# Kernel optimization log

Measured on AMD Instinct MI355X. Metric: run time of the kernel, lower is better.

Reference implementation:

```python
import jax, jax.numpy as jnp
import numpy as np

# ROIAlign config (torchvision semantics, aligned=False)
SPATIAL_SCALE = 0.25
POOLED = 7
SAMPLING_RATIO = 2
MODE = "max"  # from __init__ mode='max'


def setup_inputs() -> dict:
    key = jax.random.key(0)
    kf, kcx, kcy, kw, kh, kb = jax.random.split(key, 6)
    B, C, H, W = 2, 256, 200, 304
    N = 512
    IMG_H, IMG_W = H / SPATIAL_SCALE, W / SPATIAL_SCALE
    feature = jax.random.normal(kf, (B, C, H, W), dtype=jnp.float32)
    cx = jax.random.uniform(kcx, (N,)) * IMG_W
    cy = jax.random.uniform(kcy, (N,)) * IMG_H
    bw = jax.random.uniform(kw, (N,)) * 192.0 + 16.0
    bh = jax.random.uniform(kh, (N,)) * 192.0 + 16.0
    x1 = jnp.clip(cx - bw * 0.5, 0.0, IMG_W - 2.0)
    y1 = jnp.clip(cy - bh * 0.5, 0.0, IMG_H - 2.0)
    x2 = jnp.clip(cx + bw * 0.5, x1 + 1.0, IMG_W - 1.0)
    y2 = jnp.clip(cy + bh * 0.5, y1 + 1.0, IMG_H - 1.0)
    boxes = jnp.stack([x1, y1, x2, y2], axis=1).astype(jnp.float32)
    batch_idx = jax.random.randint(kb, (N,), 0, B, dtype=jnp.int32)
    return {"feature": feature, "boxes": boxes, "batch_idx": batch_idx}


def _sample_coords(start, size):
    # start,size: [N]; returns [N, POOLED*SAMPLING_RATIO] sample coordinates
    bin_sz = size / POOLED                         # [N]
    p = jnp.arange(POOLED, dtype=jnp.float32)      # bin index
    s = (jnp.arange(SAMPLING_RATIO, dtype=jnp.float32) + 0.5) / SAMPLING_RATIO
    # coord = start + (p + s) * bin_sz  -> [N, POOLED, RATIO]
    c = start[:, None, None] + (p[None, :, None] + s[None, None, :]) * bin_sz[:, None, None]
    return c.reshape(c.shape[0], POOLED * SAMPLING_RATIO)


def roi_align(feature, boxes, batch_idx):
    B, C, H, W = feature.shape
    roi = boxes * SPATIAL_SCALE                    # [N,4] in feature coords
    rs_x, rs_y, re_x, re_y = roi[:, 0], roi[:, 1], roi[:, 2], roi[:, 3]
    roi_w = jnp.maximum(re_x - rs_x, 1.0)
    roi_h = jnp.maximum(re_y - rs_y, 1.0)
    ys = _sample_coords(rs_y, roi_h)               # [N, Sy]
    xs = _sample_coords(rs_x, roi_w)               # [N, Sx]
    y = jnp.broadcast_to(ys[:, :, None], (ys.shape[0], ys.shape[1], xs.shape[1]))
    x = jnp.broadcast_to(xs[:, None, :], y.shape)  # [N, Sy, Sx]

    valid = (y > -1.0) & (y < H) & (x > -1.0) & (x < W)
    y = jnp.clip(y, 0.0, H - 1)
    x = jnp.clip(x, 0.0, W - 1)
    y0 = jnp.floor(y).astype(jnp.int32)
    x0 = jnp.floor(x).astype(jnp.int32)
    y1 = jnp.minimum(y0 + 1, H - 1)
    x1 = jnp.minimum(x0 + 1, W - 1)
    ly = y - y0.astype(y.dtype)
    lx = x - x0.astype(x.dtype)
    hy, hx = 1.0 - ly, 1.0 - lx
    b = batch_idx[:, None, None]
    # advanced indexing -> [N, Sy, Sx, C]
    val = (hy * hx)[..., None] * feature[b, :, y0, x0] \
        + (hy * lx)[..., None] * feature[b, :, y0, x1] \
        + (ly * hx)[..., None] * feature[b, :, y1, x0] \
        + (ly * lx)[..., None] * feature[b, :, y1, x1]
    val = jnp.where(valid[..., None], val, 0.0)
    N = boxes.shape[0]
    val = val.reshape(N, POOLED, SAMPLING_RATIO, POOLED, SAMPLING_RATIO, C)
    if MODE == "max":
        out = val.max(axis=(2, 4))                 # [N, PH, PW, C]
    else:
        out = val.mean(axis=(2, 4))
    return jnp.transpose(out, (0, 3, 1, 2))        # [N, C, PH, PW]


def reference(feature, boxes, batch_idx):
    return roi_align(feature, boxes, batch_idx)
```

## Files before the change

kernel.cpp:

```cpp
#include <hip/hip_runtime.h>


#define SPATIAL_SCALE 0.25f
#define POOLED 7
#define SR 2

constexpr int Bc = 2;
constexpr int Cc = 256;
constexpr int Hc = 200;
constexpr int Wc = 304;
constexpr int Nc = 512;

constexpr int CG      = 4;
constexpr int NSAMP   = POOLED * SR;
constexpr int NROW    = NSAMP * 2;
constexpr int XW      = 64;
constexpr int XPAD    = 68;
constexpr int CH_STR  = NROW * XPAD;
constexpr int CELLS   = POOLED * POOLED;
constexpr int OUTS    = CG * CELLS;
constexpr int PER_BOX = Cc * CELLS;
constexpr int PLANE   = Hc * Wc;

__global__ __launch_bounds__(256) void roi_align_max_kernel(
    const float* __restrict__ feature,
    const float* __restrict__ boxes,
    const int*   __restrict__ batch_idx,
    float*       __restrict__ out)
{
    __shared__ float lds[CG * CH_STR];

    int bid = blockIdx.x;
    int cg  = bid / Nc;
    int n   = bid - cg * Nc;
    int tid = threadIdx.x;

    float rsx = boxes[n * 4 + 0] * SPATIAL_SCALE;
    float rsy = boxes[n * 4 + 1] * SPATIAL_SCALE;
    float rex = boxes[n * 4 + 2] * SPATIAL_SCALE;
    float rey = boxes[n * 4 + 3] * SPATIAL_SCALE;
    float roi_w = fmaxf(rex - rsx, 1.0f);
    float roi_h = fmaxf(rey - rsy, 1.0f);
    float bin_w = roi_w / (float)POOLED;
    float bin_h = roi_h / (float)POOLED;
    int b = batch_idx[n];

    float x_first = __fadd_rn(rsx, __fmul_rn(0.25f, bin_w));
    float xc0 = fminf(fmaxf(x_first, 0.0f), (float)(Wc - 1));
    int xbase = ((int)floorf(xc0)) & ~3;

    const float* __restrict__ gbase =
        feature + ((size_t)b * Cc + (size_t)cg * CG) * (size_t)PLANE;

    int lane16 = tid & 15;
    int rbase  = tid >> 4;
    #pragma unroll
    for (int it = 0; it < 7; ++it) {
        int r       = it * 16 + rbase;
        int c_local = r / NROW;
        int slot    = r - c_local * NROW;
        int s       = slot >> 1;
        int which   = slot & 1;
        int p       = s >> 1;
        int sub     = s & 1;
        float py = (float)p + ((float)sub + 0.5f) * 0.5f;
        float fy = __fadd_rn(rsy, __fmul_rn(py, bin_h));
        float fyc = fminf(fmaxf(fy, 0.0f), (float)(Hc - 1));
        int y0 = (int)floorf(fyc);
        int row = which ? min(y0 + 1, Hc - 1) : y0;

        int col = xbase + lane16 * 4;
        col = min(col, Wc - 4);
        const float4 v = *(const float4*)(gbase + (size_t)c_local * PLANE
                                          + row * Wc + col);
        *(float4*)&lds[c_local * CH_STR + slot * XPAD + lane16 * 4] = v;
    }
    __syncthreads();

    if (tid < OUTS) {
        int c_local = tid / CELLS;
        int cell    = tid - c_local * CELLS;
        int ph      = cell / POOLED;
        int pw      = cell - ph * POOLED;
        const float* __restrict__ L = &lds[c_local * CH_STR];

        float m = -INFINITY;
        #pragma unroll
        for (int sy = 0; sy < SR; ++sy) {
            int sY = ph * SR + sy;
            float py = (float)ph + ((float)sy + 0.5f) * 0.5f;
            float fy = __fadd_rn(rsy, __fmul_rn(py, bin_h));
            bool vy = (fy > -1.0f) && (fy < (float)Hc);
            float fyc = fminf(fmaxf(fy, 0.0f), (float)(Hc - 1));
            int y0 = (int)floorf(fyc);
            float ly = fyc - (float)y0;
            float hy = 1.0f - ly;
            const float* __restrict__ r0 = L + (2 * sY) * XPAD;
            const float* __restrict__ r1 = L + (2 * sY + 1) * XPAD;

            #pragma unroll
            for (int sx = 0; sx < SR; ++sx) {
                float px = (float)pw + ((float)sx + 0.5f) * 0.5f;
                float fx = __fadd_rn(rsx, __fmul_rn(px, bin_w));
                bool vx = (fx > -1.0f) && (fx < (float)Wc);
                float fxc = fminf(fmaxf(fx, 0.0f), (float)(Wc - 1));
                int x0 = (int)floorf(fxc);
                float lx = fxc - (float)x0;
                float hx = 1.0f - lx;
                int c0 = x0 - xbase;
                int x1 = min(x0 + 1, Wc - 1);
                int c1 = x1 - xbase;

                float v00 = r0[c0], v01 = r0[c1];
                float v10 = r1[c0], v11 = r1[c1];
                float bil = hy * hx * v00 + hy * lx * v01 +
                            ly * hx * v10 + ly * lx * v11;
                float v = (vy && vx) ? bil : 0.0f;
                m = fmaxf(m, v);
            }
        }
        out[(size_t)n * PER_BOX + cg * OUTS + tid] = m;
    }
}

extern "C" void kernel_launch(void* const* d_in, const int* in_sizes, int n_in,
                              void* d_out, int out_size, void* d_ws, size_t ws_size,
                              hipStream_t stream) {
    const float* feature   = (const float*)d_in[0];
    const float* boxes     = (const float*)d_in[1];
    const int*   batch_idx = (const int*)d_in[2];
    float*       out       = (float*)d_out;

    int grid = (Cc / CG) * Nc;
    roi_align_max_kernel<<<grid, 256, 0, stream>>>(feature, boxes, batch_idx, out);
}
```

Before: 228.5 us.

## Loop channel groups per block with register-prefetched feature rows and precomputed weights

Each block now handles one box across 8 channel groups in a loop instead of one channel group, cutting the grid from one block per (box, channel group) to one per (box, chunk). The next group's feature rows are prefetched into registers while the current group is reduced from shared memory. Per-thread bilinear weights, validity masks and shared-memory addresses are computed once and reused across groups. Outputs use nontemporal stores. The gains come from amortising box setup and overlapping global loads with compute, at the cost of more registers, fewer blocks and an extra barrier per iteration.

```diff
diff --git a/kernel.cpp b/kernel.cpp
--- a/kernel.cpp
+++ b/kernel.cpp
@@ -21,6 +21,9 @@
 constexpr int OUTS    = CG * CELLS;
 constexpr int PER_BOX = Cc * CELLS;
 constexpr int PLANE   = Hc * Wc;
+constexpr int NCHUNK  = 8;
+constexpr int JITER   = (Cc / CG) / NCHUNK;
+constexpr int JSTEP_PLANES = NCHUNK * CG;
 
 __global__ __launch_bounds__(256) void roi_align_max_kernel(
     const float* __restrict__ feature,
@@ -30,96 +33,138 @@
 {
     __shared__ float lds[CG * CH_STR];
 
-    int bid = blockIdx.x;
-    int cg  = bid / Nc;
-    int n   = bid - cg * Nc;
-    int tid = threadIdx.x;
+    const int bid   = blockIdx.x;
+    const int chunk = bid & (NCHUNK - 1);
+    const int n     = bid >> 3;
+    const int tid   = threadIdx.x;
 
-    float rsx = boxes[n * 4 + 0] * SPATIAL_SCALE;
-    float rsy = boxes[n * 4 + 1] * SPATIAL_SCALE;
-    float rex = boxes[n * 4 + 2] * SPATIAL_SCALE;
-    float rey = boxes[n * 4 + 3] * SPATIAL_SCALE;
-    float roi_w = fmaxf(rex - rsx, 1.0f);
-    float roi_h = fmaxf(rey - rsy, 1.0f);
-    float bin_w = roi_w / (float)POOLED;
-    float bin_h = roi_h / (float)POOLED;
-    int b = batch_idx[n];
+    const float rsx = boxes[n * 4 + 0] * SPATIAL_SCALE;
+    const float rsy = boxes[n * 4 + 1] * SPATIAL_SCALE;
+    const float rex = boxes[n * 4 + 2] * SPATIAL_SCALE;
+    const float rey = boxes[n * 4 + 3] * SPATIAL_SCALE;
+    const float roi_w = fmaxf(rex - rsx, 1.0f);
+    const float roi_h = fmaxf(rey - rsy, 1.0f);
+    const float bin_w = roi_w / (float)POOLED;
+    const float bin_h = roi_h / (float)POOLED;
+    const int   b     = batch_idx[n];
 
-    float x_first = __fadd_rn(rsx, __fmul_rn(0.25f, bin_w));
-    float xc0 = fminf(fmaxf(x_first, 0.0f), (float)(Wc - 1));
-    int xbase = ((int)floorf(xc0)) & ~3;
+    const float x_first = __fadd_rn(rsx, __fmul_rn(0.25f, bin_w));
+    const float xc0     = fminf(fmaxf(x_first, 0.0f), (float)(Wc - 1));
+    const int   xbase   = ((int)floorf(xc0)) & ~3;
 
-    const float* __restrict__ gbase =
-        feature + ((size_t)b * Cc + (size_t)cg * CG) * (size_t)PLANE;
+    const int c_st   = tid >> 6;
+    const int lane   = tid & 63;
+    const int lane16 = lane & 15;
+    const int rquad  = lane >> 4;
 
-    int lane16 = tid & 15;
-    int rbase  = tid >> 4;
+    int g_off[7];
     #pragma unroll
     for (int it = 0; it < 7; ++it) {
-        int r       = it * 16 + rbase;
-        int c_local = r / NROW;
-        int slot    = r - c_local * NROW;
-        int s       = slot >> 1;
-        int which   = slot & 1;
-        int p       = s >> 1;
-        int sub     = s & 1;
-        float py = (float)p + ((float)sub + 0.5f) * 0.5f;
-        float fy = __fadd_rn(rsy, __fmul_rn(py, bin_h));
-        float fyc = fminf(fmaxf(fy, 0.0f), (float)(Hc - 1));
-        int y0 = (int)floorf(fyc);
-        int row = which ? min(y0 + 1, Hc - 1) : y0;
-
+        const int slot  = it * 4 + rquad;
+        const int s     = slot % NSAMP;
+        const int which = slot / NSAMP;
+        const int p     = s >> 1;
+        const int sub   = s & 1;
+        const float py  = (float)p + ((float)sub + 0.5f) * 0.5f;
+        const float fy  = __fadd_rn(rsy, __fmul_rn(py, bin_h));
+        const float fyc = fminf(fmaxf(fy, 0.0f), (float)(Hc - 1));
+        const int   y0  = (int)floorf(fyc);
+        const int   row = which ? min(y0 + 1, Hc - 1) : y0;
         int col = xbase + lane16 * 4;
         col = min(col, Wc - 4);
-        const float4 v = *(const float4*)(gbase + (size_t)c_local * PLANE
-                                          + row * Wc + col);
-        *(float4*)&lds[c_local * CH_STR + slot * XPAD + lane16 * 4] = v;
+        g_off[it] = row * Wc + col;
     }
-    __syncthreads();
+    const int lw = c_st * CH_STR + rquad * XPAD + lane16 * 4;
 
-    if (tid < OUTS) {
-        int c_local = tid / CELLS;
-        int cell    = tid - c_local * CELLS;
-        int ph      = cell / POOLED;
-        int pw      = cell - ph * POOLED;
-        const float* __restrict__ L = &lds[c_local * CH_STR];
+    const float* gp = feature
+        + ((size_t)b * Cc + (size_t)chunk * CG + c_st) * (size_t)PLANE;
 
-        float m = -INFINITY;
+    const bool has_out = (tid < OUTS);
+    float w00[2][2], w01[2][2], w10[2][2], w11[2][2];
+    int   adr[2][2][2];
+    float* outp = nullptr;
+
+    if (has_out) {
+        const int c_cl = tid / CELLS;
+        const int cell = tid - c_cl * CELLS;
+        const int ph   = cell / POOLED;
+        const int pw   = cell - ph * POOLED;
+
         #pragma unroll
         for (int sy = 0; sy < SR; ++sy) {
-            int sY = ph * SR + sy;
-            float py = (float)ph + ((float)sy + 0.5f) * 0.5f;
-            float fy = __fadd_rn(rsy, __fmul_rn(py, bin_h));
-            bool vy = (fy > -1.0f) && (fy < (float)Hc);
-            float fyc = fminf(fmaxf(fy, 0.0f), (float)(Hc - 1));
-            int y0 = (int)floorf(fyc);
-            float ly = fyc - (float)y0;
-            float hy = 1.0f - ly;
-            const float* __restrict__ r0 = L + (2 * sY) * XPAD;
-            const float* __restrict__ r1 = L + (2 * sY + 1) * XPAD;
+            const int   sY  = ph * SR + sy;
+            const float py  = (float)ph + ((float)sy + 0.5f) * 0.5f;
+            const float fy  = __fadd_rn(rsy, __fmul_rn(py, bin_h));
+            const bool  vy  = (fy > -1.0f) && (fy < (float)Hc);
+            const float fyc = fminf(fmaxf(fy, 0.0f), (float)(Hc - 1));
+            const int   y0i = (int)floorf(fyc);
+            const float ly  = fyc - (float)y0i;
+            const float hy  = 1.0f - ly;
 
             #pragma unroll
             for (int sx = 0; sx < SR; ++sx) {
-                float px = (float)pw + ((float)sx + 0.5f) * 0.5f;
-                float fx = __fadd_rn(rsx, __fmul_rn(px, bin_w));
-                bool vx = (fx > -1.0f) && (fx < (float)Wc);
-                float fxc = fminf(fmaxf(fx, 0.0f), (float)(Wc - 1));
-                int x0 = (int)floorf(fxc);
-                float lx = fxc - (float)x0;
-                float hx = 1.0f - lx;
-                int c0 = x0 - xbase;
-                int x1 = min(x0 + 1, Wc - 1);
-                int c1 = x1 - xbase;
-
-                float v00 = r0[c0], v01 = r0[c1];
-                float v10 = r1[c0], v11 = r1[c1];
-                float bil = hy * hx * v00 + hy * lx * v01 +
-                            ly * hx * v10 + ly * lx * v11;
-                float v = (vy && vx) ? bil : 0.0f;
-                m = fmaxf(m, v);
+                const float px  = (float)pw + ((float)sx + 0.5f) * 0.5f;
+                const float fx  = __fadd_rn(rsx, __fmul_rn(px, bin_w));
+                const bool  vx  = (fx > -1.0f) && (fx < (float)Wc);
+                const float fxc = fminf(fmaxf(fx, 0.0f), (float)(Wc - 1));
+                const int   x0i = (int)floorf(fxc);
+                const float lx  = fxc - (float)x0i;
+                const float hx  = 1.0f - lx;
+                const int   c0  = x0i - xbase;
+                const bool  v   = vy && vx;
+                w00[sy][sx] = v ? hy * hx : 0.0f;
+                w01[sy][sx] = v ? hy * lx : 0.0f;
+                w10[sy][sx] = v ? ly * hx : 0.0f;
+                w11[sy][sx] = v ? ly * lx : 0.0f;
+                adr[sy][0][sx] = c_cl * CH_STR + sY * XPAD + c0;
+                adr[sy][1][sx] = c_cl * CH_STR + (sY + NSAMP) * XPAD + c0;
             }
         }
-        out[(size_t)n * PER_BOX + cg * OUTS + tid] = m;
+        outp = out + (size_t)n * PER_BOX
+                   + ((size_t)chunk * CG + c_cl) * CELLS + cell;
+    }
+
+    float4 st[7];
+    #pragma unroll
+    for (int it = 0; it < 7; ++it)
+        st[it] = *(const float4*)(gp + g_off[it]);
+
+    for (int j = 0; j < JITER; ++j) {
+        #pragma unroll
+        for (int it = 0; it < 7; ++it)
+            *(float4*)&lds[lw + it * (4 * XPAD)] = st[it];
+
+        if (j + 1 < JITER) {
+            gp += (size_t)JSTEP_PLANES * PLANE;
+            #pragma unroll
+            for (int it = 0; it < 7; ++it)
+                st[it] = *(const float4*)(gp + g_off[it]);
+        }
+
+        __syncthreads();
+
+        if (has_out) {
+            float m = -INFINITY;
+            #pragma unroll
+            for (int sy = 0; sy < SR; ++sy) {
+                #pragma unroll
+                for (int sx = 0; sx < SR; ++sx) {
+                    const int a0 = adr[sy][0][sx];
+                    const int a1 = adr[sy][1][sx];
+                    const float v00 = lds[a0];
+                    const float v01 = lds[a0 + 1];
+                    const float v10 = lds[a1];
+                    const float v11 = lds[a1 + 1];
+                    const float bil = w00[sy][sx] * v00 + w01[sy][sx] * v01
+                                    + w10[sy][sx] * v10 + w11[sy][sx] * v11;
+                    m = fmaxf(m, bil);
+                }
+            }
+            __builtin_nontemporal_store(m, outp);
+            outp += NCHUNK * CG * CELLS;
+        }
+
+        __syncthreads();
     }
 }
 
@@ -131,6 +176,6 @@
     const int*   batch_idx = (const int*)d_in[2];
     float*       out       = (float*)d_out;
 
-    int grid = (Cc / CG) * Nc;
+    int grid = Nc * NCHUNK;
     roi_align_max_kernel<<<grid, 256, 0, stream>>>(feature, boxes, batch_idx, out);
 }
```

After: 513.5 us. +124.7%, slower.

## Precompute per-ROI bilinear weights and LDS offsets in a separate kernel

Applied to the files above, without the earlier changes.

Adds a small precompute kernel that writes, for each box, the bilinear weights (with the validity mask folded in), the LDS tap offsets, the row offsets and xbase into a workspace table. The main kernel reads this table instead of recomputing the coordinates in every one of the 64 channel-group blocks per box. It also restructures the staging loads so each thread issues all 7 global float4 loads before any LDS stores, and changes the LDS row layout. The cost is an extra kernel launch and table reads, and the workspace must be large enough, otherwise a fallback kernel runs.

```diff
diff --git a/kernel.cpp b/kernel.cpp
--- a/kernel.cpp
+++ b/kernel.cpp
@@ -14,7 +14,6 @@
 constexpr int CG      = 4;
 constexpr int NSAMP   = POOLED * SR;
 constexpr int NROW    = NSAMP * 2;
-constexpr int XW      = 64;
 constexpr int XPAD    = 68;
 constexpr int CH_STR  = NROW * XPAD;
 constexpr int CELLS   = POOLED * POOLED;
@@ -22,7 +21,160 @@
 constexpr int PER_BOX = Cc * CELLS;
 constexpr int PLANE   = Hc * Wc;
 
-__global__ __launch_bounds__(256) void roi_align_max_kernel(
+constexpr int TB_F  = 1216;
+constexpr int A_OFF = 784;
+constexpr int R_OFF = 1176;
+constexpr int X_OFF = 1204;
+constexpr size_t TABLE_BYTES = (size_t)Nc * TB_F * sizeof(float);
+
+__global__ __launch_bounds__(64) void roi_precompute_kernel(
+    const float* __restrict__ boxes,
+    float*       __restrict__ table)
+{
+    const int n   = blockIdx.x;
+    const int tid = threadIdx.x;
+
+    const float rsx = boxes[n * 4 + 0] * SPATIAL_SCALE;
+    const float rsy = boxes[n * 4 + 1] * SPATIAL_SCALE;
+    const float rex = boxes[n * 4 + 2] * SPATIAL_SCALE;
+    const float rey = boxes[n * 4 + 3] * SPATIAL_SCALE;
+    const float roi_w = fmaxf(rex - rsx, 1.0f);
+    const float roi_h = fmaxf(rey - rsy, 1.0f);
+    const float bin_w = roi_w / (float)POOLED;
+    const float bin_h = roi_h / (float)POOLED;
+    const float x_first = __fadd_rn(rsx, __fmul_rn(0.25f, bin_w));
+    const float xc0     = fminf(fmaxf(x_first, 0.0f), (float)(Wc - 1));
+    const int   xbase   = ((int)floorf(xc0)) & ~3;
+
+    float* tb = table + (size_t)n * TB_F;
+    int*   ti = (int*)tb;
+
+    if (tid < CELLS) {
+        const int ph = tid / POOLED;
+        const int pw = tid - ph * POOLED;
+        #pragma unroll
+        for (int sy = 0; sy < SR; ++sy) {
+            const int   sY  = ph * SR + sy;
+            const float py  = (float)ph + ((float)sy + 0.5f) * 0.5f;
+            const float fy  = __fadd_rn(rsy, __fmul_rn(py, bin_h));
+            const bool  vy  = (fy > -1.0f) && (fy < (float)Hc);
+            const float fyc = fminf(fmaxf(fy, 0.0f), (float)(Hc - 1));
+            const int   y0i = (int)floorf(fyc);
+            const float ly  = fyc - (float)y0i;
+            const float hy  = 1.0f - ly;
+            #pragma unroll
+            for (int sx = 0; sx < SR; ++sx) {
+                const float px  = (float)pw + ((float)sx + 0.5f) * 0.5f;
+                const float fx  = __fadd_rn(rsx, __fmul_rn(px, bin_w));
+                const bool  vx  = (fx > -1.0f) && (fx < (float)Wc);
+                const float fxc = fminf(fmaxf(fx, 0.0f), (float)(Wc - 1));
+                const int   x0i = (int)floorf(fxc);
+                const float lx  = fxc - (float)x0i;
+                const float hx  = 1.0f - lx;
+                const int   c0  = x0i - xbase;
+                const bool  v   = vy && vx;
+                float4 w;
+                w.x = v ? hy * hx : 0.0f;
+                w.y = v ? hy * lx : 0.0f;
+                w.z = v ? ly * hx : 0.0f;
+                w.w = v ? ly * lx : 0.0f;
+                const int tap = sy * SR + sx;
+                ((float4*)tb)[tid * 4 + tap] = w;
+                ti[A_OFF + tid * 8 + tap * 2 + 0] = sY * XPAD + c0;
+                ti[A_OFF + tid * 8 + tap * 2 + 1] = (NSAMP + sY) * XPAD + c0;
+            }
+        }
+    }
+    if (tid < NROW) {
+        const int which = tid / NSAMP;
+        const int s     = tid - which * NSAMP;
+        const int p     = s >> 1;
+        const int sub   = s & 1;
+        const float py  = (float)p + ((float)sub + 0.5f) * 0.5f;
+        const float fy  = __fadd_rn(rsy, __fmul_rn(py, bin_h));
+        const float fyc = fminf(fmaxf(fy, 0.0f), (float)(Hc - 1));
+        const int   y0  = (int)floorf(fyc);
+        const int   row = which ? min(y0 + 1, Hc - 1) : y0;
+        ti[R_OFF + tid] = row * Wc;
+    }
+    if (tid == 0) ti[X_OFF] = xbase;
+}
+
+__global__ __launch_bounds__(256) void roi_align_main_kernel(
+    const float* __restrict__ feature,
+    const int*   __restrict__ batch_idx,
+    const float* __restrict__ table,
+    float*       __restrict__ out)
+{
+    __shared__ float lds[CG * CH_STR];
+
+    const int bid = blockIdx.x;
+    const int cg  = bid / Nc;
+    const int n   = bid - cg * Nc;
+    const int tid = threadIdx.x;
+
+    const float* tb = table + (size_t)n * TB_F;
+    const int*   ti = (const int*)tb;
+
+    const int b     = batch_idx[n];
+    const int xbase = ti[X_OFF];
+
+    const int c_st   = tid >> 6;
+    const int lane16 = tid & 15;
+    const int rquad  = (tid >> 4) & 3;
+    const int col    = min(xbase + lane16 * 4, Wc - 4);
+
+    int roff[7];
+    #pragma unroll
+    for (int it = 0; it < 7; ++it)
+        roff[it] = ti[R_OFF + it * 4 + rquad];
+
+    const int cellc = min(tid, OUTS - 1);
+    const int c_cl  = cellc / CELLS;
+    const int cell  = cellc - c_cl * CELLS;
+    const float4* wp = (const float4*)tb + (size_t)cell * 4;
+    const float4 wv0 = wp[0], wv1 = wp[1], wv2 = wp[2], wv3 = wp[3];
+    const int4* ap = (const int4*)(ti + A_OFF) + (size_t)cell * 2;
+    const int4 av0 = ap[0], av1 = ap[1];
+
+    const float* __restrict__ gbase =
+        feature + ((size_t)b * Cc + (size_t)cg * CG + c_st) * (size_t)PLANE;
+    float4 st[7];
+    #pragma unroll
+    for (int it = 0; it < 7; ++it)
+        st[it] = *(const float4*)(gbase + roff[it] + col);
+
+    const int lw = c_st * CH_STR + rquad * XPAD + lane16 * 4;
+    #pragma unroll
+    for (int it = 0; it < 7; ++it)
+        *(float4*)&lds[lw + it * (4 * XPAD)] = st[it];
+
+    __syncthreads();
+
+    if (tid < OUTS) {
+        const int lbase = c_cl * CH_STR;
+        float m = -INFINITY;
+        {   const int a0 = av0.x + lbase, a1 = av0.y + lbase;
+            const float bil = wv0.x * lds[a0] + wv0.y * lds[a0 + 1]
+                            + wv0.z * lds[a1] + wv0.w * lds[a1 + 1];
+            m = fmaxf(m, bil); }
+        {   const int a0 = av0.z + lbase, a1 = av0.w + lbase;
+            const float bil = wv1.x * lds[a0] + wv1.y * lds[a0 + 1]
+                            + wv1.z * lds[a1] + wv1.w * lds[a1 + 1];
+            m = fmaxf(m, bil); }
+        {   const int a0 = av1.x + lbase, a1 = av1.y + lbase;
+            const float bil = wv2.x * lds[a0] + wv2.y * lds[a0 + 1]
+                            + wv2.z * lds[a1] + wv2.w * lds[a1 + 1];
+            m = fmaxf(m, bil); }
+        {   const int a0 = av1.z + lbase, a1 = av1.w + lbase;
+            const float bil = wv3.x * lds[a0] + wv3.y * lds[a0 + 1]
+                            + wv3.z * lds[a1] + wv3.w * lds[a1 + 1];
+            m = fmaxf(m, bil); }
+        out[(size_t)n * PER_BOX + cg * OUTS + tid] = m;
+    }
+}
+
+__global__ __launch_bounds__(256) void roi_align_max_fallback(
     const float* __restrict__ feature,
     const float* __restrict__ boxes,
     const int*   __restrict__ batch_idx,
@@ -59,8 +211,8 @@
         int r       = it * 16 + rbase;
         int c_local = r / NROW;
         int slot    = r - c_local * NROW;
-        int s       = slot >> 1;
-        int which   = slot & 1;
+        int s       = slot % NSAMP;
+        int which   = slot / NSAMP;
         int p       = s >> 1;
         int sub     = s & 1;
         float py = (float)p + ((float)sub + 0.5f) * 0.5f;
@@ -68,11 +220,9 @@
         float fyc = fminf(fmaxf(fy, 0.0f), (float)(Hc - 1));
         int y0 = (int)floorf(fyc);
         int row = which ? min(y0 + 1, Hc - 1) : y0;
-
-        int col = xbase + lane16 * 4;
-        col = min(col, Wc - 4);
+        int colf = min(xbase + lane16 * 4, Wc - 4);
         const float4 v = *(const float4*)(gbase + (size_t)c_local * PLANE
-                                          + row * Wc + col);
+                                          + row * Wc + colf);
         *(float4*)&lds[c_local * CH_STR + slot * XPAD + lane16 * 4] = v;
     }
     __syncthreads();
@@ -95,8 +245,8 @@
             int y0 = (int)floorf(fyc);
             float ly = fyc - (float)y0;
             float hy = 1.0f - ly;
-            const float* __restrict__ r0 = L + (2 * sY) * XPAD;
-            const float* __restrict__ r1 = L + (2 * sY + 1) * XPAD;
+            const float* __restrict__ r0 = L + sY * XPAD;
+            const float* __restrict__ r1 = L + (NSAMP + sY) * XPAD;
 
             #pragma unroll
             for (int sx = 0; sx < SR; ++sx) {
@@ -108,11 +258,9 @@
                 float lx = fxc - (float)x0;
                 float hx = 1.0f - lx;
                 int c0 = x0 - xbase;
-                int x1 = min(x0 + 1, Wc - 1);
-                int c1 = x1 - xbase;
-
-                float v00 = r0[c0], v01 = r0[c1];
-                float v10 = r1[c0], v11 = r1[c1];
+
+                float v00 = r0[c0], v01 = r0[c0 + 1];
+                float v10 = r1[c0], v11 = r1[c0 + 1];
                 float bil = hy * hx * v00 + hy * lx * v01 +
                             ly * hx * v10 + ly * lx * v11;
                 float v = (vy && vx) ? bil : 0.0f;
@@ -131,6 +279,14 @@
     const int*   batch_idx = (const int*)d_in[2];
     float*       out       = (float*)d_out;
 
-    int grid = (Cc / CG) * Nc;
-    roi_align_max_kernel<<<grid, 256, 0, stream>>>(feature, boxes, batch_idx, out);
-}
+    const int grid = (Cc / CG) * Nc;
+    if (d_ws != nullptr && ws_size >= TABLE_BYTES) {
+        float* table = (float*)d_ws;
+        roi_precompute_kernel<<<Nc, 64, 0, stream>>>(boxes, table);
+        roi_align_main_kernel<<<grid, 256, 0, stream>>>(feature, batch_idx,
+                                                        table, out);
+    } else {
+        roi_align_max_fallback<<<grid, 256, 0, stream>>>(feature, boxes,
+                                                         batch_idx, out);
+    }
+}
```

After: 255.4 us. +11.8%, slower.
